# Optimization experiments

Measured on AMD Instinct MI355X. Metric: run time of the kernel, lower is better.

## Reference

```python
import jax, jax.numpy as jnp
import numpy as np

N_NODES = 100352
NUM_GRAPHS = 512
NODES_PER_GRAPH = 196  # N_NODES / NUM_GRAPHS, equal-size graphs
N_EDGES = 1605632
IN_C, HID_C, OUT_C, K = 128, 64, 32, 30


def setup_inputs() -> dict:
    key = jax.random.key(0)
    ks = jax.random.split(key, 4)
    x = jax.random.normal(ks[0], (N_NODES, IN_C), dtype=jnp.float32)
    edge_index = jax.random.randint(ks[1], (2, N_EDGES), 0, N_NODES, dtype=jnp.int32)
    batch = jnp.repeat(jnp.arange(NUM_GRAPHS, dtype=jnp.int32), NODES_PER_GRAPH)
    W1 = jax.random.normal(ks[2], (IN_C, HID_C), jnp.float32) * (1.0 / np.sqrt(IN_C))
    b1 = jnp.zeros((HID_C,), jnp.float32)
    W2 = jax.random.normal(ks[3], (HID_C, OUT_C), jnp.float32) * (1.0 / np.sqrt(HID_C))
    b2 = jnp.zeros((OUT_C,), jnp.float32)
    return dict(x=x, edge_index=edge_index, batch=batch, W1=W1, b1=b1, W2=W2, b2=b2)


def gcn_conv(x, src, dst, W, b, num_nodes):
    # PyG GCNConv: xW, add self-loops, symmetric normalization, scatter-add to dst.
    xw = x @ W  # [N, D_out]
    deg = jax.ops.segment_sum(jnp.ones_like(dst, dtype=xw.dtype), dst,
                              num_segments=num_nodes) + 1.0  # +1 for self-loop
    dis = jax.lax.rsqrt(deg)  # deg^{-1/2}
    msg = (dis[src] * dis[dst])[:, None] * xw[src]  # [E, D_out]
    out = jax.ops.segment_sum(msg, dst, num_segments=num_nodes)
    out = out + (dis * dis)[:, None] * xw  # self-loop term deg^{-1} * xw
    return out + b


def sort_pool(x, batch, num_graphs, max_nodes, k):
    # PyG SortAggregation: dense per-graph batch, sort nodes desc by last channel, top-k, zero padding.
    N, D = x.shape
    fill = x.min() - 1.0
    counts = jax.ops.segment_sum(jnp.ones((N,), jnp.int32), batch, num_segments=num_graphs)
    starts = jnp.cumsum(counts) - counts  # exclusive prefix sum
    pos = jnp.arange(N, dtype=jnp.int32) - starts[batch]
    dense = jnp.full((num_graphs, max_nodes, D), fill, x.dtype).at[batch, pos].set(x)
    order = jnp.argsort(-dense[:, :, -1], axis=1)[:, :k]  # [B, k] top-k by last channel
    topk = jnp.take_along_axis(dense, order[:, :, None], axis=1)  # [B, k, D]
    topk = jnp.where(topk == fill, jnp.zeros((), x.dtype), topk)
    return topk.reshape(num_graphs, k * D)


def reference(x, edge_index, batch, W1, b1, W2, b2):
    src, dst = edge_index[0], edge_index[1]
    n = x.shape[0]
    h = jax.nn.relu(gcn_conv(x, src, dst, W1, b1, n))
    h = gcn_conv(h, src, dst, W2, b2, n)
    return sort_pool(h, batch, NUM_GRAPHS, NODES_PER_GRAPH, K)
```

## Files before the change

kernel.cpp:

```cpp
#include <hip/hip_runtime.h>

#define N_NODES   100352
#define N_EDGES   1605632
#define IN_C      128
#define HID_C     64
#define OUT_C     32
#define NUM_GRAPHS 512
#define NPG       196
#define TOPK      30

#define NB        196
#define BCAP      10240
#define LCAP      10240

typedef float v16f __attribute__((ext_vector_type(16)));

#define OFF_DEG     0u
#define OFF_ROWPTR  401408u
#define OFF_DIS     802816u
#define OFF_BCNT    1204224u
#define OFF_ARENA   1206272u
#define OFF_OUT2    1206272u
#define OFF_CSR     17262592u
#define OFF_XW1     23685120u
#define OFF_H       49375232u
#define OFF_XW2     75065344u

__global__ __launch_bounds__(256) void k_bucket(const int* __restrict__ src, const int* __restrict__ dst,
                                                int* __restrict__ bucket_cnt, int* __restrict__ arena) {
    __shared__ int hist[NB];
    __shared__ int cur[NB];
    int tid = threadIdx.x;
    for (int i = tid; i < NB; i += 256) hist[i] = 0;
    __syncthreads();
    int e0 = (blockIdx.x * 256 + tid) * 8;
    int4 sa = ((const int4*)src)[e0 / 4], sb = ((const int4*)src)[e0 / 4 + 1];
    int4 da = ((const int4*)dst)[e0 / 4], db = ((const int4*)dst)[e0 / 4 + 1];
    int es[8] = {sa.x, sa.y, sa.z, sa.w, sb.x, sb.y, sb.z, sb.w};
    int ed[8] = {da.x, da.y, da.z, da.w, db.x, db.y, db.z, db.w};
    int eb[8];
#pragma unroll
    for (int j = 0; j < 8; ++j) { eb[j] = ed[j] >> 9; atomicAdd(&hist[eb[j]], 1); }
    __syncthreads();
    for (int i = tid; i < NB; i += 256) {
        int c = hist[i];
        cur[i] = (c > 0) ? atomicAdd(&bucket_cnt[i], c) : 0;
    }
    __syncthreads();
#pragma unroll
    for (int j = 0; j < 8; ++j) {
        int p = atomicAdd(&cur[eb[j]], 1);
        if (p < BCAP) arena[(size_t)eb[j] * BCAP + p] = (es[j] << 9) | (ed[j] & 511);
    }
}

__global__ __launch_bounds__(256) void k_build(const int* __restrict__ arena, const int* __restrict__ bucket_cnt,
                                               int* __restrict__ row_ptr,
                                               int* __restrict__ deg, float* __restrict__ dis,
                                               int* __restrict__ csr_src) {
    __shared__ int bsc[256];
    __shared__ int dloc[512];
    __shared__ int sc[512];
    __shared__ int cur[512];
    __shared__ int stage[LCAP];
    int b = blockIdx.x;
    int tid = threadIdx.x;
    int bv = (tid < NB) ? bucket_cnt[tid] : 0;
    bsc[tid] = bv;
    __syncthreads();
    for (int o = 1; o < 256; o <<= 1) {
        int a = (tid >= o) ? bsc[tid - o] : 0;
        __syncthreads();
        bsc[tid] += a;
        __syncthreads();
    }
    int nb = min(bucket_cnt[b], BCAP);
    int gbase = bsc[b] - bucket_cnt[b];
    const int* ap = arena + (size_t)b * BCAP;
    for (int i = tid; i < 512; i += 256) dloc[i] = 0;
    __syncthreads();
    for (int i = tid; i < nb; i += 256) {
        int e = ap[i];
        atomicAdd(&dloc[e & 511], 1);
    }
    __syncthreads();
    for (int i = tid; i < 512; i += 256) sc[i] = dloc[i];
    __syncthreads();
    for (int o = 1; o < 512; o <<= 1) {
        int i0 = tid, i1 = tid + 256;
        int v0 = (i0 >= o) ? sc[i0 - o] : 0;
        int v1 = (i1 >= o) ? sc[i1 - o] : 0;
        __syncthreads();
        sc[i0] += v0;
        sc[i1] += v1;
        __syncthreads();
    }
    for (int i = tid; i < 512; i += 256) {
        int d = dloc[i];
        int off = sc[i] - d;
        int node = b * 512 + i;
        row_ptr[node] = gbase + off;
        deg[node] = d;
        dis[node] = (float)(1.0 / sqrt((double)(d + 1)));
        cur[i] = off;
    }
    __syncthreads();
    bool inlds = (nb <= LCAP);
    for (int i = tid; i < nb; i += 256) {
        int e = ap[i];
        int p = atomicAdd(&cur[e & 511], 1);
        int sv = ((unsigned)e) >> 9;
        if (inlds) stage[p] = sv;
        else       csr_src[gbase + p] = sv;
    }
    __syncthreads();
    if (inlds)
        for (int i = tid; i < nb; i += 256) csr_src[gbase + i] = stage[i];
}

__global__ __launch_bounds__(256) void k_mm1(const float* __restrict__ x, const float* __restrict__ W1,
                                             const float* __restrict__ dis, float* __restrict__ xw1s) {
    int tid = threadIdx.x;
    int n = blockIdx.x * 64 + (tid & 63);
    int ch = __builtin_amdgcn_readfirstlane((tid >> 6) * 16);
    const float4* xrow = (const float4*)(x + (size_t)n * IN_C);
    float acc[16];
#pragma unroll
    for (int c = 0; c < 16; ++c) acc[c] = 0.f;
    float4 xq = xrow[0];
#pragma unroll 1
    for (int q = 0; q < IN_C / 4; ++q) {
        float4 xn = xrow[(q + 1) & (IN_C / 4 - 1)];
        const float* wp = W1 + q * 4 * HID_C + ch;
        v16f w0, w1, w2, w3;
        asm volatile("s_load_dwordx16 %0, %1, 0x0"   : "=s"(w0) : "s"(wp));
        asm volatile("s_load_dwordx16 %0, %1, 0x100" : "=s"(w1) : "s"(wp));
        asm volatile("s_load_dwordx16 %0, %1, 0x200" : "=s"(w2) : "s"(wp));
        asm volatile("s_load_dwordx16 %0, %1, 0x300" : "=s"(w3) : "s"(wp));
        asm volatile("s_waitcnt lgkmcnt(0)" : "+s"(w0), "+s"(w1), "+s"(w2), "+s"(w3));
#pragma unroll
        for (int c = 0; c < 16; ++c) {
            acc[c] = fmaf(xq.x, w0[c], acc[c]);
            acc[c] = fmaf(xq.y, w1[c], acc[c]);
            acc[c] = fmaf(xq.z, w2[c], acc[c]);
            acc[c] = fmaf(xq.w, w3[c], acc[c]);
        }
        xq = xn;
    }
    float dv = dis[n];
    float4* orow = (float4*)(xw1s + (size_t)n * HID_C + ch);
#pragma unroll
    for (int c4 = 0; c4 < 4; ++c4) {
        float4 o;
        o.x = acc[4 * c4 + 0] * dv;
        o.y = acc[4 * c4 + 1] * dv;
        o.z = acc[4 * c4 + 2] * dv;
        o.w = acc[4 * c4 + 3] * dv;
        orow[c4] = o;
    }
}

__global__ __launch_bounds__(256) void k_agg1(const float* __restrict__ xw1s, const int* __restrict__ csr_src,
                                              const int* __restrict__ row_ptr, const int* __restrict__ deg,
                                              const float* __restrict__ dis, const float* __restrict__ b1,
                                              float* __restrict__ h) {
    int lane = threadIdx.x & 63;
    int v = blockIdx.x * 4 + (threadIdx.x >> 6);
    int start = row_ptr[v];
    int cnt = deg[v];
    float acc0 = xw1s[(size_t)v * HID_C + lane];
    float acc1 = 0.f, acc2 = 0.f, acc3 = 0.f;
    for (int base = 0; base < cnt; base += 64) {
        int mcnt = min(64, cnt - base);
        int sj = 0;
        if (lane < mcnt) sj = csr_src[start + base + lane];
        int j = 0;
        for (; j + 8 <= mcnt; j += 8) {
            int s0 = __shfl(sj, j + 0), s1 = __shfl(sj, j + 1);
            int s2 = __shfl(sj, j + 2), s3 = __shfl(sj, j + 3);
            int s4 = __shfl(sj, j + 4), s5 = __shfl(sj, j + 5);
            int s6 = __shfl(sj, j + 6), s7 = __shfl(sj, j + 7);
            float v0 = xw1s[(size_t)s0 * HID_C + lane];
            float v1 = xw1s[(size_t)s1 * HID_C + lane];
            float v2 = xw1s[(size_t)s2 * HID_C + lane];
            float v3 = xw1s[(size_t)s3 * HID_C + lane];
            float v4 = xw1s[(size_t)s4 * HID_C + lane];
            float v5 = xw1s[(size_t)s5 * HID_C + lane];
            float v6 = xw1s[(size_t)s6 * HID_C + lane];
            float v7 = xw1s[(size_t)s7 * HID_C + lane];
            acc0 += v0 + v4;
            acc1 += v1 + v5;
            acc2 += v2 + v6;
            acc3 += v3 + v7;
        }
        for (; j < mcnt; ++j) {
            int s = __shfl(sj, j);
            acc0 += xw1s[(size_t)s * HID_C + lane];
        }
    }
    float o = fmaf(dis[v], (acc0 + acc1) + (acc2 + acc3), b1[lane]);
    h[(size_t)v * HID_C + lane] = fmaxf(o, 0.f);
}

__global__ __launch_bounds__(256) void k_mm2(const float* __restrict__ h, const float* __restrict__ W2,
                                             const float* __restrict__ dis, float* __restrict__ xw2s) {
    int tid = threadIdx.x;
    int n = blockIdx.x * 128 + (tid & 127);
    int ch = __builtin_amdgcn_readfirstlane((tid >> 7) * 16);
    const float4* hrow = (const float4*)(h + (size_t)n * HID_C);
    float acc[16];
#pragma unroll
    for (int c = 0; c < 16; ++c) acc[c] = 0.f;
    float4 xq = hrow[0];
#pragma unroll 1
    for (int q = 0; q < HID_C / 4; ++q) {
        float4 xn = hrow[(q + 1) & (HID_C / 4 - 1)];
        const float* wp = W2 + q * 4 * OUT_C + ch;
        v16f w0, w1, w2, w3;
        asm volatile("s_load_dwordx16 %0, %1, 0x0"   : "=s"(w0) : "s"(wp));
        asm volatile("s_load_dwordx16 %0, %1, 0x80"  : "=s"(w1) : "s"(wp));
        asm volatile("s_load_dwordx16 %0, %1, 0x100" : "=s"(w2) : "s"(wp));
        asm volatile("s_load_dwordx16 %0, %1, 0x180" : "=s"(w3) : "s"(wp));
        asm volatile("s_waitcnt lgkmcnt(0)" : "+s"(w0), "+s"(w1), "+s"(w2), "+s"(w3));
#pragma unroll
        for (int c = 0; c < 16; ++c) {
            acc[c] = fmaf(xq.x, w0[c], acc[c]);
            acc[c] = fmaf(xq.y, w1[c], acc[c]);
            acc[c] = fmaf(xq.z, w2[c], acc[c]);
            acc[c] = fmaf(xq.w, w3[c], acc[c]);
        }
        xq = xn;
    }
    float dv = dis[n];
    float4* orow = (float4*)(xw2s + (size_t)n * OUT_C + ch);
#pragma unroll
    for (int c4 = 0; c4 < 4; ++c4) {
        float4 o;
        o.x = acc[4 * c4 + 0] * dv;
        o.y = acc[4 * c4 + 1] * dv;
        o.z = acc[4 * c4 + 2] * dv;
        o.w = acc[4 * c4 + 3] * dv;
        orow[c4] = o;
    }
}

__global__ __launch_bounds__(256) void k_agg2(const float* __restrict__ xw2s, const int* __restrict__ csr_src,
                                              const int* __restrict__ row_ptr, const int* __restrict__ deg,
                                              const float* __restrict__ dis, const float* __restrict__ b2,
                                              float* __restrict__ out2) {
    int lane = threadIdx.x & 31;
    int v = blockIdx.x * 8 + (threadIdx.x >> 5);
    int start = row_ptr[v];
    int cnt = deg[v];
    float acc0 = xw2s[(size_t)v * OUT_C + lane];
    float acc1 = 0.f, acc2 = 0.f, acc3 = 0.f;
    for (int base = 0; base < cnt; base += 32) {
        int mcnt = min(32, cnt - base);
        int sj = 0;
        if (lane < mcnt) sj = csr_src[start + base + lane];
        int j = 0;
        for (; j + 8 <= mcnt; j += 8) {
            int s0 = __shfl(sj, j + 0, 32), s1 = __shfl(sj, j + 1, 32);
            int s2 = __shfl(sj, j + 2, 32), s3 = __shfl(sj, j + 3, 32);
            int s4 = __shfl(sj, j + 4, 32), s5 = __shfl(sj, j + 5, 32);
            int s6 = __shfl(sj, j + 6, 32), s7 = __shfl(sj, j + 7, 32);
            float v0 = xw2s[(size_t)s0 * OUT_C + lane];
            float v1 = xw2s[(size_t)s1 * OUT_C + lane];
            float v2 = xw2s[(size_t)s2 * OUT_C + lane];
            float v3 = xw2s[(size_t)s3 * OUT_C + lane];
            float v4 = xw2s[(size_t)s4 * OUT_C + lane];
            float v5 = xw2s[(size_t)s5 * OUT_C + lane];
            float v6 = xw2s[(size_t)s6 * OUT_C + lane];
            float v7 = xw2s[(size_t)s7 * OUT_C + lane];
            acc0 += v0 + v4;
            acc1 += v1 + v5;
            acc2 += v2 + v6;
            acc3 += v3 + v7;
        }
        for (; j < mcnt; ++j) {
            int s = __shfl(sj, j, 32);
            acc0 += xw2s[(size_t)s * OUT_C + lane];
        }
    }
    out2[(size_t)v * OUT_C + lane] = fmaf(dis[v], (acc0 + acc1) + (acc2 + acc3), b2[lane]);
}

__global__ __launch_bounds__(256) void k_sort(const float* __restrict__ out2, float* __restrict__ out) {
    __shared__ float keys[NPG];
    __shared__ int order[TOPK];
    int g = blockIdx.x;
    int tid = threadIdx.x;
    int base = g * NPG;
    if (tid < NPG) keys[tid] = out2[(size_t)(base + tid) * OUT_C + (OUT_C - 1)];
    __syncthreads();
    if (tid < NPG) {
        float my = keys[tid];
        int r = 0;
        for (int j = 0; j < NPG; ++j) {
            float kj = keys[j];
            r += (kj > my) || (kj == my && j < tid);
        }
        if (r < TOPK) order[r] = tid;
    }
    __syncthreads();
    for (int idx = tid; idx < TOPK * OUT_C; idx += 256) {
        int r = idx >> 5;
        int c = idx & 31;
        int n = order[r];
        out[g * (TOPK * OUT_C) + idx] = out2[(size_t)(base + n) * OUT_C + c];
    }
}

extern "C" void kernel_launch(void* const* d_in, const int* in_sizes, int n_in,
                              void* d_out, int out_size, void* d_ws, size_t ws_size,
                              hipStream_t stream) {
    const float* x  = (const float*)d_in[0];
    const int*   ei = (const int*)d_in[1];
    const int*   srcp = ei;
    const int*   dstp = ei + N_EDGES;
    const float* W1 = (const float*)d_in[3];
    const float* b1 = (const float*)d_in[4];
    const float* W2 = (const float*)d_in[5];
    const float* b2 = (const float*)d_in[6];
    float* out = (float*)d_out;

    char* w = (char*)d_ws;
    int*    deg      = (int*)(w + OFF_DEG);
    int*    row_ptr  = (int*)(w + OFF_ROWPTR);
    float*  dis      = (float*)(w + OFF_DIS);
    int*    bcnt     = (int*)(w + OFF_BCNT);
    int*    arena    = (int*)(w + OFF_ARENA);
    int*    csr_src  = (int*)(w + OFF_CSR);
    float*  xw1s     = (float*)(w + OFF_XW1);
    float*  h        = (float*)(w + OFF_H);
    float*  xw2s     = (float*)(w + OFF_XW2);
    float*  out2     = (float*)(w + OFF_OUT2);

    hipMemsetAsync(bcnt, 0, NB * sizeof(int), stream);
    k_bucket<<<N_EDGES / (256 * 8), 256, 0, stream>>>(srcp, dstp, bcnt, arena);
    k_build <<<NB, 256, 0, stream>>>(arena, bcnt, row_ptr, deg, dis, csr_src);
    k_mm1   <<<N_NODES / 64, 256, 0, stream>>>(x, W1, dis, xw1s);
    k_agg1  <<<N_NODES / 4, 256, 0, stream>>>(xw1s, csr_src, row_ptr, deg, dis, b1, h);
    k_mm2   <<<N_NODES / 128, 256, 0, stream>>>(h, W2, dis, xw2s);
    k_agg2  <<<N_NODES / 8, 256, 0, stream>>>(xw2s, csr_src, row_ptr, deg, dis, b2, out2);
    k_sort  <<<NUM_GRAPHS, 256, 0, stream>>>(out2, out);
}
```

Baseline: 220.7 us.

## Fuse edge bucketing with first matmul and move source scaling into aggregation

The edge bucketing kernel and the first x@W1 matmul are merged into one launch with a block-index split, so the dense matmul can overlap the atomic-heavy bucketing. This is possible because the matmul no longer depends on the degree normalisation: the per-source dis factor is now applied inside agg1 by gathering dis[src] per edge. Both aggregation loops are also unrolled from 8 to 16 gathers in flight. The cost is an extra dis gather and shuffle per edge in agg1, plus higher register pressure from the wider unroll.

```diff
diff --git a/kernel.cpp b/kernel.cpp
--- a/kernel.cpp
+++ b/kernel.cpp
@@ -12,6 +12,7 @@
 #define NB        196
 #define BCAP      10240
 #define LCAP      10240
+#define NBUCKET_BLOCKS 784
 
 typedef float v16f __attribute__((ext_vector_type(16)));
 
@@ -26,31 +27,73 @@
 #define OFF_H       49375232u
 #define OFF_XW2     75065344u
 
-__global__ __launch_bounds__(256) void k_bucket(const int* __restrict__ src, const int* __restrict__ dst,
-                                                int* __restrict__ bucket_cnt, int* __restrict__ arena) {
-    __shared__ int hist[NB];
-    __shared__ int cur[NB];
+__global__ __launch_bounds__(256) void k_phase1(const int* __restrict__ src, const int* __restrict__ dst,
+                                                int* __restrict__ bucket_cnt, int* __restrict__ arena,
+                                                const float* __restrict__ x, const float* __restrict__ W1,
+                                                float* __restrict__ xw1) {
     int tid = threadIdx.x;
-    for (int i = tid; i < NB; i += 256) hist[i] = 0;
-    __syncthreads();
-    int e0 = (blockIdx.x * 256 + tid) * 8;
-    int4 sa = ((const int4*)src)[e0 / 4], sb = ((const int4*)src)[e0 / 4 + 1];
-    int4 da = ((const int4*)dst)[e0 / 4], db = ((const int4*)dst)[e0 / 4 + 1];
-    int es[8] = {sa.x, sa.y, sa.z, sa.w, sb.x, sb.y, sb.z, sb.w};
-    int ed[8] = {da.x, da.y, da.z, da.w, db.x, db.y, db.z, db.w};
-    int eb[8];
-#pragma unroll
-    for (int j = 0; j < 8; ++j) { eb[j] = ed[j] >> 9; atomicAdd(&hist[eb[j]], 1); }
-    __syncthreads();
-    for (int i = tid; i < NB; i += 256) {
-        int c = hist[i];
-        cur[i] = (c > 0) ? atomicAdd(&bucket_cnt[i], c) : 0;
-    }
-    __syncthreads();
-#pragma unroll
-    for (int j = 0; j < 8; ++j) {
-        int p = atomicAdd(&cur[eb[j]], 1);
-        if (p < BCAP) arena[(size_t)eb[j] * BCAP + p] = (es[j] << 9) | (ed[j] & 511);
+    if (blockIdx.x < NBUCKET_BLOCKS) {
+        __shared__ int hist[NB];
+        __shared__ int cur[NB];
+        for (int i = tid; i < NB; i += 256) hist[i] = 0;
+        __syncthreads();
+        int e0 = (blockIdx.x * 256 + tid) * 8;
+        int4 sa = ((const int4*)src)[e0 / 4], sb = ((const int4*)src)[e0 / 4 + 1];
+        int4 da = ((const int4*)dst)[e0 / 4], db = ((const int4*)dst)[e0 / 4 + 1];
+        int es[8] = {sa.x, sa.y, sa.z, sa.w, sb.x, sb.y, sb.z, sb.w};
+        int ed[8] = {da.x, da.y, da.z, da.w, db.x, db.y, db.z, db.w};
+        int eb[8];
+#pragma unroll
+        for (int j = 0; j < 8; ++j) { eb[j] = ed[j] >> 9; atomicAdd(&hist[eb[j]], 1); }
+        __syncthreads();
+        for (int i = tid; i < NB; i += 256) {
+            int c = hist[i];
+            cur[i] = (c > 0) ? atomicAdd(&bucket_cnt[i], c) : 0;
+        }
+        __syncthreads();
+#pragma unroll
+        for (int j = 0; j < 8; ++j) {
+            int p = atomicAdd(&cur[eb[j]], 1);
+            if (p < BCAP) arena[(size_t)eb[j] * BCAP + p] = (es[j] << 9) | (ed[j] & 511);
+        }
+    } else {
+        int bid = blockIdx.x - NBUCKET_BLOCKS;
+        int n = bid * 64 + (tid & 63);
+        int ch = __builtin_amdgcn_readfirstlane((tid >> 6) * 16);
+        const float4* xrow = (const float4*)(x + (size_t)n * IN_C);
+        float acc[16];
+#pragma unroll
+        for (int c = 0; c < 16; ++c) acc[c] = 0.f;
+        float4 xq = xrow[0];
+#pragma unroll 1
+        for (int q = 0; q < IN_C / 4; ++q) {
+            float4 xn = xrow[(q + 1) & (IN_C / 4 - 1)];
+            const float* wp = W1 + q * 4 * HID_C + ch;
+            v16f w0, w1, w2, w3;
+            asm volatile("s_load_dwordx16 %0, %1, 0x0"   : "=s"(w0) : "s"(wp));
+            asm volatile("s_load_dwordx16 %0, %1, 0x100" : "=s"(w1) : "s"(wp));
+            asm volatile("s_load_dwordx16 %0, %1, 0x200" : "=s"(w2) : "s"(wp));
+            asm volatile("s_load_dwordx16 %0, %1, 0x300" : "=s"(w3) : "s"(wp));
+            asm volatile("s_waitcnt lgkmcnt(0)" : "+s"(w0), "+s"(w1), "+s"(w2), "+s"(w3));
+#pragma unroll
+            for (int c = 0; c < 16; ++c) {
+                acc[c] = fmaf(xq.x, w0[c], acc[c]);
+                acc[c] = fmaf(xq.y, w1[c], acc[c]);
+                acc[c] = fmaf(xq.z, w2[c], acc[c]);
+                acc[c] = fmaf(xq.w, w3[c], acc[c]);
+            }
+            xq = xn;
+        }
+        float4* orow = (float4*)(xw1 + (size_t)n * HID_C + ch);
+#pragma unroll
+        for (int c4 = 0; c4 < 4; ++c4) {
+            float4 o;
+            o.x = acc[4 * c4 + 0];
+            o.y = acc[4 * c4 + 1];
+            o.z = acc[4 * c4 + 2];
+            o.w = acc[4 * c4 + 3];
+            orow[c4] = o;
+        }
     }
 }
 
@@ -118,49 +161,7 @@
         for (int i = tid; i < nb; i += 256) csr_src[gbase + i] = stage[i];
 }
 
-__global__ __launch_bounds__(256) void k_mm1(const float* __restrict__ x, const float* __restrict__ W1,
-                                             const float* __restrict__ dis, float* __restrict__ xw1s) {
-    int tid = threadIdx.x;
-    int n = blockIdx.x * 64 + (tid & 63);
-    int ch = __builtin_amdgcn_readfirstlane((tid >> 6) * 16);
-    const float4* xrow = (const float4*)(x + (size_t)n * IN_C);
-    float acc[16];
-#pragma unroll
-    for (int c = 0; c < 16; ++c) acc[c] = 0.f;
-    float4 xq = xrow[0];
-#pragma unroll 1
-    for (int q = 0; q < IN_C / 4; ++q) {
-        float4 xn = xrow[(q + 1) & (IN_C / 4 - 1)];
-        const float* wp = W1 + q * 4 * HID_C + ch;
-        v16f w0, w1, w2, w3;
-        asm volatile("s_load_dwordx16 %0, %1, 0x0"   : "=s"(w0) : "s"(wp));
-        asm volatile("s_load_dwordx16 %0, %1, 0x100" : "=s"(w1) : "s"(wp));
-        asm volatile("s_load_dwordx16 %0, %1, 0x200" : "=s"(w2) : "s"(wp));
-        asm volatile("s_load_dwordx16 %0, %1, 0x300" : "=s"(w3) : "s"(wp));
-        asm volatile("s_waitcnt lgkmcnt(0)" : "+s"(w0), "+s"(w1), "+s"(w2), "+s"(w3));
-#pragma unroll
-        for (int c = 0; c < 16; ++c) {
-            acc[c] = fmaf(xq.x, w0[c], acc[c]);
-            acc[c] = fmaf(xq.y, w1[c], acc[c]);
-            acc[c] = fmaf(xq.z, w2[c], acc[c]);
-            acc[c] = fmaf(xq.w, w3[c], acc[c]);
-        }
-        xq = xn;
-    }
-    float dv = dis[n];
-    float4* orow = (float4*)(xw1s + (size_t)n * HID_C + ch);
-#pragma unroll
-    for (int c4 = 0; c4 < 4; ++c4) {
-        float4 o;
-        o.x = acc[4 * c4 + 0] * dv;
-        o.y = acc[4 * c4 + 1] * dv;
-        o.z = acc[4 * c4 + 2] * dv;
-        o.w = acc[4 * c4 + 3] * dv;
-        orow[c4] = o;
-    }
-}
-
-__global__ __launch_bounds__(256) void k_agg1(const float* __restrict__ xw1s, const int* __restrict__ csr_src,
+__global__ __launch_bounds__(256) void k_agg1(const float* __restrict__ xw1, const int* __restrict__ csr_src,
                                               const int* __restrict__ row_ptr, const int* __restrict__ deg,
                                               const float* __restrict__ dis, const float* __restrict__ b1,
                                               float* __restrict__ h) {
@@ -168,37 +169,47 @@
     int v = blockIdx.x * 4 + (threadIdx.x >> 6);
     int start = row_ptr[v];
     int cnt = deg[v];
-    float acc0 = xw1s[(size_t)v * HID_C + lane];
+    float dv = dis[v];
+    float acc0 = dv * xw1[(size_t)v * HID_C + lane];
     float acc1 = 0.f, acc2 = 0.f, acc3 = 0.f;
     for (int base = 0; base < cnt; base += 64) {
         int mcnt = min(64, cnt - base);
-        int sj = 0;
-        if (lane < mcnt) sj = csr_src[start + base + lane];
+        int sj = 0; float dj = 0.f;
+        if (lane < mcnt) { sj = csr_src[start + base + lane]; dj = dis[sj]; }
         int j = 0;
-        for (; j + 8 <= mcnt; j += 8) {
-            int s0 = __shfl(sj, j + 0), s1 = __shfl(sj, j + 1);
-            int s2 = __shfl(sj, j + 2), s3 = __shfl(sj, j + 3);
-            int s4 = __shfl(sj, j + 4), s5 = __shfl(sj, j + 5);
-            int s6 = __shfl(sj, j + 6), s7 = __shfl(sj, j + 7);
-            float v0 = xw1s[(size_t)s0 * HID_C + lane];
-            float v1 = xw1s[(size_t)s1 * HID_C + lane];
-            float v2 = xw1s[(size_t)s2 * HID_C + lane];
-            float v3 = xw1s[(size_t)s3 * HID_C + lane];
-            float v4 = xw1s[(size_t)s4 * HID_C + lane];
-            float v5 = xw1s[(size_t)s5 * HID_C + lane];
-            float v6 = xw1s[(size_t)s6 * HID_C + lane];
-            float v7 = xw1s[(size_t)s7 * HID_C + lane];
-            acc0 += v0 + v4;
-            acc1 += v1 + v5;
-            acc2 += v2 + v6;
-            acc3 += v3 + v7;
+        for (; j + 16 <= mcnt; j += 16) {
+            int   s0 = __shfl(sj, j + 0),  s1 = __shfl(sj, j + 1),  s2 = __shfl(sj, j + 2),  s3 = __shfl(sj, j + 3);
+            int   s4 = __shfl(sj, j + 4),  s5 = __shfl(sj, j + 5),  s6 = __shfl(sj, j + 6),  s7 = __shfl(sj, j + 7);
+            int   s8 = __shfl(sj, j + 8),  s9 = __shfl(sj, j + 9),  sA = __shfl(sj, j + 10), sB = __shfl(sj, j + 11);
+            int   sC = __shfl(sj, j + 12), sD = __shfl(sj, j + 13), sE = __shfl(sj, j + 14), sF = __shfl(sj, j + 15);
+            float d0 = __shfl(dj, j + 0),  d1 = __shfl(dj, j + 1),  d2 = __shfl(dj, j + 2),  d3 = __shfl(dj, j + 3);
+            float d4 = __shfl(dj, j + 4),  d5 = __shfl(dj, j + 5),  d6 = __shfl(dj, j + 6),  d7 = __shfl(dj, j + 7);
+            float d8 = __shfl(dj, j + 8),  d9 = __shfl(dj, j + 9),  dA = __shfl(dj, j + 10), dB = __shfl(dj, j + 11);
+            float dC = __shfl(dj, j + 12), dD = __shfl(dj, j + 13), dE = __shfl(dj, j + 14), dF = __shfl(dj, j + 15);
+            float v0 = xw1[(size_t)s0 * HID_C + lane], v1 = xw1[(size_t)s1 * HID_C + lane];
+            float v2 = xw1[(size_t)s2 * HID_C + lane], v3 = xw1[(size_t)s3 * HID_C + lane];
+            float v4 = xw1[(size_t)s4 * HID_C + lane], v5 = xw1[(size_t)s5 * HID_C + lane];
+            float v6 = xw1[(size_t)s6 * HID_C + lane], v7 = xw1[(size_t)s7 * HID_C + lane];
+            float v8 = xw1[(size_t)s8 * HID_C + lane], v9 = xw1[(size_t)s9 * HID_C + lane];
+            float vA = xw1[(size_t)sA * HID_C + lane], vB = xw1[(size_t)sB * HID_C + lane];
+            float vC = xw1[(size_t)sC * HID_C + lane], vD = xw1[(size_t)sD * HID_C + lane];
+            float vE = xw1[(size_t)sE * HID_C + lane], vF = xw1[(size_t)sF * HID_C + lane];
+            acc0 = fmaf(d0, v0, acc0); acc1 = fmaf(d1, v1, acc1);
+            acc2 = fmaf(d2, v2, acc2); acc3 = fmaf(d3, v3, acc3);
+            acc0 = fmaf(d4, v4, acc0); acc1 = fmaf(d5, v5, acc1);
+            acc2 = fmaf(d6, v6, acc2); acc3 = fmaf(d7, v7, acc3);
+            acc0 = fmaf(d8, v8, acc0); acc1 = fmaf(d9, v9, acc1);
+            acc2 = fmaf(dA, vA, acc2); acc3 = fmaf(dB, vB, acc3);
+            acc0 = fmaf(dC, vC, acc0); acc1 = fmaf(dD, vD, acc1);
+            acc2 = fmaf(dE, vE, acc2); acc3 = fmaf(dF, vF, acc3);
         }
         for (; j < mcnt; ++j) {
             int s = __shfl(sj, j);
-            acc0 += xw1s[(size_t)s * HID_C + lane];
-        }
-    }
-    float o = fmaf(dis[v], (acc0 + acc1) + (acc2 + acc3), b1[lane]);
+            float d = __shfl(dj, j);
+            acc0 = fmaf(d, xw1[(size_t)s * HID_C + lane], acc0);
+        }
+    }
+    float o = fmaf(dv, (acc0 + acc1) + (acc2 + acc3), b1[lane]);
     h[(size_t)v * HID_C + lane] = fmaxf(o, 0.f);
 }
 
@@ -259,23 +270,25 @@
         int sj = 0;
         if (lane < mcnt) sj = csr_src[start + base + lane];
         int j = 0;
-        for (; j + 8 <= mcnt; j += 8) {
-            int s0 = __shfl(sj, j + 0, 32), s1 = __shfl(sj, j + 1, 32);
-            int s2 = __shfl(sj, j + 2, 32), s3 = __shfl(sj, j + 3, 32);
-            int s4 = __shfl(sj, j + 4, 32), s5 = __shfl(sj, j + 5, 32);
-            int s6 = __shfl(sj, j + 6, 32), s7 = __shfl(sj, j + 7, 32);
-            float v0 = xw2s[(size_t)s0 * OUT_C + lane];
-            float v1 = xw2s[(size_t)s1 * OUT_C + lane];
-            float v2 = xw2s[(size_t)s2 * OUT_C + lane];
-            float v3 = xw2s[(size_t)s3 * OUT_C + lane];
-            float v4 = xw2s[(size_t)s4 * OUT_C + lane];
-            float v5 = xw2s[(size_t)s5 * OUT_C + lane];
-            float v6 = xw2s[(size_t)s6 * OUT_C + lane];
-            float v7 = xw2s[(size_t)s7 * OUT_C + lane];
-            acc0 += v0 + v4;
-            acc1 += v1 + v5;
-            acc2 += v2 + v6;
-            acc3 += v3 + v7;
+        for (; j + 16 <= mcnt; j += 16) {
+            int s0 = __shfl(sj, j + 0, 32),  s1 = __shfl(sj, j + 1, 32);
+            int s2 = __shfl(sj, j + 2, 32),  s3 = __shfl(sj, j + 3, 32);
+            int s4 = __shfl(sj, j + 4, 32),  s5 = __shfl(sj, j + 5, 32);
+            int s6 = __shfl(sj, j + 6, 32),  s7 = __shfl(sj, j + 7, 32);
+            int s8 = __shfl(sj, j + 8, 32),  s9 = __shfl(sj, j + 9, 32);
+            int sA = __shfl(sj, j + 10, 32), sB = __shfl(sj, j + 11, 32);
+            int sC = __shfl(sj, j + 12, 32), sD = __shfl(sj, j + 13, 32);
+            int sE = __shfl(sj, j + 14, 32), sF = __shfl(sj, j + 15, 32);
+            float v0 = xw2s[(size_t)s0 * OUT_C + lane], v1 = xw2s[(size_t)s1 * OUT_C + lane];
+            float v2 = xw2s[(size_t)s2 * OUT_C + lane], v3 = xw2s[(size_t)s3 * OUT_C + lane];
+            float v4 = xw2s[(size_t)s4 * OUT_C + lane], v5 = xw2s[(size_t)s5 * OUT_C + lane];
+            float v6 = xw2s[(size_t)s6 * OUT_C + lane], v7 = xw2s[(size_t)s7 * OUT_C + lane];
+            float v8 = xw2s[(size_t)s8 * OUT_C + lane], v9 = xw2s[(size_t)s9 * OUT_C + lane];
+            float vA = xw2s[(size_t)sA * OUT_C + lane], vB = xw2s[(size_t)sB * OUT_C + lane];
+            float vC = xw2s[(size_t)sC * OUT_C + lane], vD = xw2s[(size_t)sD * OUT_C + lane];
+            float vE = xw2s[(size_t)sE * OUT_C + lane], vF = xw2s[(size_t)sF * OUT_C + lane];
+            acc0 += v0 + v4; acc1 += v1 + v5; acc2 += v2 + v6; acc3 += v3 + v7;
+            acc0 += v8 + vC; acc1 += v9 + vD; acc2 += vA + vE; acc3 += vB + vF;
         }
         for (; j < mcnt; ++j) {
             int s = __shfl(sj, j, 32);
@@ -331,16 +344,15 @@
     int*    bcnt     = (int*)(w + OFF_BCNT);
     int*    arena    = (int*)(w + OFF_ARENA);
     int*    csr_src  = (int*)(w + OFF_CSR);
-    float*  xw1s     = (float*)(w + OFF_XW1);
+    float*  xw1      = (float*)(w + OFF_XW1);
     float*  h        = (float*)(w + OFF_H);
     float*  xw2s     = (float*)(w + OFF_XW2);
     float*  out2     = (float*)(w + OFF_OUT2);
 
     hipMemsetAsync(bcnt, 0, NB * sizeof(int), stream);
-    k_bucket<<<N_EDGES / (256 * 8), 256, 0, stream>>>(srcp, dstp, bcnt, arena);
+    k_phase1<<<NBUCKET_BLOCKS + N_NODES / 64, 256, 0, stream>>>(srcp, dstp, bcnt, arena, x, W1, xw1);
     k_build <<<NB, 256, 0, stream>>>(arena, bcnt, row_ptr, deg, dis, csr_src);
-    k_mm1   <<<N_NODES / 64, 256, 0, stream>>>(x, W1, dis, xw1s);
-    k_agg1  <<<N_NODES / 4, 256, 0, stream>>>(xw1s, csr_src, row_ptr, deg, dis, b1, h);
+    k_agg1  <<<N_NODES / 4, 256, 0, stream>>>(xw1, csr_src, row_ptr, deg, dis, b1, h);
     k_mm2   <<<N_NODES / 128, 256, 0, stream>>>(h, W2, dis, xw2s);
     k_agg2  <<<N_NODES / 8, 256, 0, stream>>>(xw2s, csr_src, row_ptr, deg, dis, b2, out2);
     k_sort  <<<NUM_GRAPHS, 256, 0, stream>>>(out2, out);
```

Result: slower. 252.8 us (+14.5%).

## Fuse layer-2 aggregation with per-graph sort pool; widen bucket kernel per-block work

Applied to the files above, without the earlier changes.

Merges the second GCN aggregation and the sort-pool into one kernel with one 512-thread block per graph. The 196x32 output tile stays in LDS and the top-k gather reads from LDS, which removes the out2 global round trip and one launch. Separately, the edge-bucketing kernel now processes 32 edges per thread instead of 8, using fewer blocks with more atomics per block. The trade-off is only 512 blocks for the aggregation instead of 12544, which may cost latency hiding on the gathers.

```diff
diff --git a/kernel.cpp b/kernel.cpp
--- a/kernel.cpp
+++ b/kernel.cpp
@@ -20,7 +20,6 @@
 #define OFF_DIS     802816u
 #define OFF_BCNT    1204224u
 #define OFF_ARENA   1206272u
-#define OFF_OUT2    1206272u
 #define OFF_CSR     17262592u
 #define OFF_XW1     23685120u
 #define OFF_H       49375232u
@@ -33,14 +32,15 @@
     int tid = threadIdx.x;
     for (int i = tid; i < NB; i += 256) hist[i] = 0;
     __syncthreads();
-    int e0 = (blockIdx.x * 256 + tid) * 8;
-    int4 sa = ((const int4*)src)[e0 / 4], sb = ((const int4*)src)[e0 / 4 + 1];
-    int4 da = ((const int4*)dst)[e0 / 4], db = ((const int4*)dst)[e0 / 4 + 1];
-    int es[8] = {sa.x, sa.y, sa.z, sa.w, sb.x, sb.y, sb.z, sb.w};
-    int ed[8] = {da.x, da.y, da.z, da.w, db.x, db.y, db.z, db.w};
-    int eb[8];
-#pragma unroll
-    for (int j = 0; j < 8; ++j) { eb[j] = ed[j] >> 9; atomicAdd(&hist[eb[j]], 1); }
+    int base4 = blockIdx.x * 2048 + tid;
+#pragma unroll
+    for (int r = 0; r < 8; ++r) {
+        int4 d = ((const int4*)dst)[base4 + r * 256];
+        atomicAdd(&hist[d.x >> 9], 1);
+        atomicAdd(&hist[d.y >> 9], 1);
+        atomicAdd(&hist[d.z >> 9], 1);
+        atomicAdd(&hist[d.w >> 9], 1);
+    }
     __syncthreads();
     for (int i = tid; i < NB; i += 256) {
         int c = hist[i];
@@ -48,9 +48,17 @@
     }
     __syncthreads();
 #pragma unroll
-    for (int j = 0; j < 8; ++j) {
-        int p = atomicAdd(&cur[eb[j]], 1);
-        if (p < BCAP) arena[(size_t)eb[j] * BCAP + p] = (es[j] << 9) | (ed[j] & 511);
+    for (int r = 0; r < 8; ++r) {
+        int4 s = ((const int4*)src)[base4 + r * 256];
+        int4 d = ((const int4*)dst)[base4 + r * 256];
+        int p0 = atomicAdd(&cur[d.x >> 9], 1);
+        int p1 = atomicAdd(&cur[d.y >> 9], 1);
+        int p2 = atomicAdd(&cur[d.z >> 9], 1);
+        int p3 = atomicAdd(&cur[d.w >> 9], 1);
+        if (p0 < BCAP) arena[(size_t)(d.x >> 9) * BCAP + p0] = (s.x << 9) | (d.x & 511);
+        if (p1 < BCAP) arena[(size_t)(d.y >> 9) * BCAP + p1] = (s.y << 9) | (d.y & 511);
+        if (p2 < BCAP) arena[(size_t)(d.z >> 9) * BCAP + p2] = (s.z << 9) | (d.z & 511);
+        if (p3 < BCAP) arena[(size_t)(d.w >> 9) * BCAP + p3] = (s.w << 9) | (d.w & 511);
     }
 }
 
@@ -244,70 +252,70 @@
     }
 }
 
-__global__ __launch_bounds__(256) void k_agg2(const float* __restrict__ xw2s, const int* __restrict__ csr_src,
-                                              const int* __restrict__ row_ptr, const int* __restrict__ deg,
-                                              const float* __restrict__ dis, const float* __restrict__ b2,
-                                              float* __restrict__ out2) {
-    int lane = threadIdx.x & 31;
-    int v = blockIdx.x * 8 + (threadIdx.x >> 5);
-    int start = row_ptr[v];
-    int cnt = deg[v];
-    float acc0 = xw2s[(size_t)v * OUT_C + lane];
-    float acc1 = 0.f, acc2 = 0.f, acc3 = 0.f;
-    for (int base = 0; base < cnt; base += 32) {
-        int mcnt = min(32, cnt - base);
-        int sj = 0;
-        if (lane < mcnt) sj = csr_src[start + base + lane];
-        int j = 0;
-        for (; j + 8 <= mcnt; j += 8) {
-            int s0 = __shfl(sj, j + 0, 32), s1 = __shfl(sj, j + 1, 32);
-            int s2 = __shfl(sj, j + 2, 32), s3 = __shfl(sj, j + 3, 32);
-            int s4 = __shfl(sj, j + 4, 32), s5 = __shfl(sj, j + 5, 32);
-            int s6 = __shfl(sj, j + 6, 32), s7 = __shfl(sj, j + 7, 32);
-            float v0 = xw2s[(size_t)s0 * OUT_C + lane];
-            float v1 = xw2s[(size_t)s1 * OUT_C + lane];
-            float v2 = xw2s[(size_t)s2 * OUT_C + lane];
-            float v3 = xw2s[(size_t)s3 * OUT_C + lane];
-            float v4 = xw2s[(size_t)s4 * OUT_C + lane];
-            float v5 = xw2s[(size_t)s5 * OUT_C + lane];
-            float v6 = xw2s[(size_t)s6 * OUT_C + lane];
-            float v7 = xw2s[(size_t)s7 * OUT_C + lane];
-            acc0 += v0 + v4;
-            acc1 += v1 + v5;
-            acc2 += v2 + v6;
-            acc3 += v3 + v7;
-        }
-        for (; j < mcnt; ++j) {
-            int s = __shfl(sj, j, 32);
-            acc0 += xw2s[(size_t)s * OUT_C + lane];
-        }
-    }
-    out2[(size_t)v * OUT_C + lane] = fmaf(dis[v], (acc0 + acc1) + (acc2 + acc3), b2[lane]);
-}
-
-__global__ __launch_bounds__(256) void k_sort(const float* __restrict__ out2, float* __restrict__ out) {
+__global__ __launch_bounds__(512) void k_agg2sort(const float* __restrict__ xw2s, const int* __restrict__ csr_src,
+                                                  const int* __restrict__ row_ptr, const int* __restrict__ deg,
+                                                  const float* __restrict__ dis, const float* __restrict__ b2,
+                                                  float* __restrict__ out) {
+    __shared__ float o2[NPG][OUT_C];
     __shared__ float keys[NPG];
     __shared__ int order[TOPK];
     int g = blockIdx.x;
     int tid = threadIdx.x;
-    int base = g * NPG;
-    if (tid < NPG) keys[tid] = out2[(size_t)(base + tid) * OUT_C + (OUT_C - 1)];
-    __syncthreads();
-    if (tid < NPG) {
-        float my = keys[tid];
+    int lane = tid & 31;
+    int grp = tid >> 5;
+    for (int i = grp; i < NPG; i += 16) {
+        int v = g * NPG + i;
+        int start = row_ptr[v];
+        int cnt = deg[v];
+        float acc0 = xw2s[(size_t)v * OUT_C + lane];
+        float acc1 = 0.f, acc2 = 0.f, acc3 = 0.f;
+        for (int base = 0; base < cnt; base += 32) {
+            int mcnt = min(32, cnt - base);
+            int sj = 0;
+            if (lane < mcnt) sj = csr_src[start + base + lane];
+            int j = 0;
+            for (; j + 8 <= mcnt; j += 8) {
+                int s0 = __shfl(sj, j + 0, 32), s1 = __shfl(sj, j + 1, 32);
+                int s2 = __shfl(sj, j + 2, 32), s3 = __shfl(sj, j + 3, 32);
+                int s4 = __shfl(sj, j + 4, 32), s5 = __shfl(sj, j + 5, 32);
+                int s6 = __shfl(sj, j + 6, 32), s7 = __shfl(sj, j + 7, 32);
+                float v0 = xw2s[(size_t)s0 * OUT_C + lane];
+                float v1 = xw2s[(size_t)s1 * OUT_C + lane];
+                float v2 = xw2s[(size_t)s2 * OUT_C + lane];
+                float v3 = xw2s[(size_t)s3 * OUT_C + lane];
+                float v4 = xw2s[(size_t)s4 * OUT_C + lane];
+                float v5 = xw2s[(size_t)s5 * OUT_C + lane];
+                float v6 = xw2s[(size_t)s6 * OUT_C + lane];
+                float v7 = xw2s[(size_t)s7 * OUT_C + lane];
+                acc0 += v0 + v4;
+                acc1 += v1 + v5;
+                acc2 += v2 + v6;
+                acc3 += v3 + v7;
+            }
+            for (; j < mcnt; ++j) {
+                int s = __shfl(sj, j, 32);
+                acc0 += xw2s[(size_t)s * OUT_C + lane];
+            }
+        }
+        float val = fmaf(dis[v], (acc0 + acc1) + (acc2 + acc3), b2[lane]);
+        o2[i][lane] = val;
+        if (lane == OUT_C - 1) keys[i] = val;
+    }
+    __syncthreads();
+    for (int i = tid; i < NPG; i += 512) {
+        float my = keys[i];
         int r = 0;
         for (int j = 0; j < NPG; ++j) {
             float kj = keys[j];
-            r += (kj > my) || (kj == my && j < tid);
-        }
-        if (r < TOPK) order[r] = tid;
-    }
-    __syncthreads();
-    for (int idx = tid; idx < TOPK * OUT_C; idx += 256) {
+            r += (kj > my) || (kj == my && j < i);
+        }
+        if (r < TOPK) order[r] = i;
+    }
+    __syncthreads();
+    for (int idx = tid; idx < TOPK * OUT_C; idx += 512) {
         int r = idx >> 5;
         int c = idx & 31;
-        int n = order[r];
-        out[g * (TOPK * OUT_C) + idx] = out2[(size_t)(base + n) * OUT_C + c];
+        out[g * (TOPK * OUT_C) + idx] = o2[order[r]][c];
     }
 }
 
@@ -334,14 +342,12 @@
     float*  xw1s     = (float*)(w + OFF_XW1);
     float*  h        = (float*)(w + OFF_H);
     float*  xw2s     = (float*)(w + OFF_XW2);
-    float*  out2     = (float*)(w + OFF_OUT2);
 
     hipMemsetAsync(bcnt, 0, NB * sizeof(int), stream);
-    k_bucket<<<N_EDGES / (256 * 8), 256, 0, stream>>>(srcp, dstp, bcnt, arena);
+    k_bucket<<<N_EDGES / (256 * 32), 256, 0, stream>>>(srcp, dstp, bcnt, arena);
     k_build <<<NB, 256, 0, stream>>>(arena, bcnt, row_ptr, deg, dis, csr_src);
     k_mm1   <<<N_NODES / 64, 256, 0, stream>>>(x, W1, dis, xw1s);
     k_agg1  <<<N_NODES / 4, 256, 0, stream>>>(xw1s, csr_src, row_ptr, deg, dis, b1, h);
     k_mm2   <<<N_NODES / 128, 256, 0, stream>>>(h, W2, dis, xw2s);
-    k_agg2  <<<N_NODES / 8, 256, 0, stream>>>(xw2s, csr_src, row_ptr, deg, dis, b2, out2);
-    k_sort  <<<NUM_GRAPHS, 256, 0, stream>>>(out2, out);
-}
+    k_agg2sort<<<NUM_GRAPHS, 512, 0, stream>>>(xw2s, csr_src, row_ptr, deg, dis, b2, out);
+}
```

Result: no change. 224.8 us (+1.9%).
